# Performance work log

Hardware: AMD Instinct MI355X
Metric: run time of the kernel (lower is better)

## Reference

```python
import jax, jax.numpy as jnp
import numpy as np

N = 256        # total_nodes = num_instruments(16) + num_temporal_nodes(240)
D = 512        # node_dim
H = 512        # hidden_dim
E = 128        # edge_dim
HEADS = 4
L = 3          # num GAT layers
SLOPE = 0.2
LN_EPS = 1e-5


def _ln(x, g, b):
    m = jnp.mean(x, axis=-1, keepdims=True)
    v = jnp.mean((x - m) ** 2, axis=-1, keepdims=True)
    return (x - m) * jax.lax.rsqrt(v + LN_EPS) * g + b


def _pair_mlp(pairs, w1, b1, g, beta, w2, b2):
    # Linear -> LayerNorm -> LeakyReLU(0.2) -> Linear (dropout is identity in eval)
    h = pairs @ w1 + b1
    h = jax.nn.leaky_relu(_ln(h, g, beta), SLOPE)
    return h @ w2 + b2


def setup_inputs() -> dict:
    key = jax.random.key(0)
    ks = jax.random.split(key, 16)
    s = 0.02
    return {
        "emb": jax.random.normal(ks[0], (N, D), jnp.float32),
        # edge_predictor MLP: Linear(2D,H), LN(H), Linear(H,1)
        "ep_w1": jax.random.normal(ks[1], (2 * D, H), jnp.float32) * s,
        "ep_b1": jnp.zeros((H,), jnp.float32),
        "ep_g": jnp.ones((H,), jnp.float32),
        "ep_beta": jnp.zeros((H,), jnp.float32),
        "ep_w2": jax.random.normal(ks[2], (H, 1), jnp.float32) * s,
        "ep_b2": jnp.zeros((1,), jnp.float32),
        # edge_feature_net MLP: Linear(2D,H), LN(H), Linear(H,E)
        "ef_w1": jax.random.normal(ks[3], (2 * D, H), jnp.float32) * s,
        "ef_b1": jnp.zeros((H,), jnp.float32),
        "ef_g": jnp.ones((H,), jnp.float32),
        "ef_beta": jnp.zeros((H,), jnp.float32),
        "ef_w2": jax.random.normal(ks[4], (H, E), jnp.float32) * s,
        "ef_b2": jnp.zeros((E,), jnp.float32),
        # 3 GATConv layers (in=out=512, heads=4, concat=False), stacked
        "gat_W": jax.random.normal(ks[5], (L, H, HEADS * H), jnp.float32) * s,
        "gat_a_src": jax.random.normal(ks[6], (L, HEADS, H), jnp.float32) * s,
        "gat_a_dst": jax.random.normal(ks[7], (L, HEADS, H), jnp.float32) * s,
        "gat_b": jnp.zeros((L, H), jnp.float32),
        # output_proj: Linear(H,H), LN(H), Linear(H,D)
        "op_w1": jax.random.normal(ks[8], (H, H), jnp.float32) * s,
        "op_b1": jnp.zeros((H,), jnp.float32),
        "op_g": jnp.ones((H,), jnp.float32),
        "op_beta": jnp.zeros((H,), jnp.float32),
        "op_w2": jax.random.normal(ks[9], (H, D), jnp.float32) * s,
        "op_b2": jnp.zeros((D,), jnp.float32),
    }


def reference(emb, ep_w1, ep_b1, ep_g, ep_beta, ep_w2, ep_b2,
              ef_w1, ef_b1, ef_g, ef_beta, ef_w2, ef_b2,
              gat_W, gat_a_src, gat_a_dst, gat_b,
              op_w1, op_b1, op_g, op_beta, op_w2, op_b2):
    # ---- _construct_graph, fully vectorized over all ordered pairs ----
    # pairs[i, j] = concat(x_i, x_j)  -> [N, N, 2D]
    pairs = jnp.concatenate([
        jnp.broadcast_to(emb[:, None, :], (N, N, D)),
        jnp.broadcast_to(emb[None, :, :], (N, N, D)),
    ], axis=-1)
    prob = jax.nn.sigmoid(_pair_mlp(pairs, ep_w1, ep_b1, ep_g, ep_beta, ep_w2, ep_b2))[..., 0]  # [N,N]
    off_diag = ~jnp.eye(N, dtype=bool)
    active = (prob > 0.5) & off_diag           # active[i,j]: edge i -> j selected
    edge_feats = _pair_mlp(pairs, ef_w1, ef_b1, ef_g, ef_beta, ef_w2, ef_b2)  # [N,N,E]

    # adjacency in (dst, src) layout + self loops (PyG GATConv add_self_loops=True)
    adj = active.T | jnp.eye(N, dtype=bool)    # adj[dst, src]

    # ---- GATConv stack (heads=4, concat=False -> mean over heads) ----
    x = emb
    for l in range(L):
        s = (x @ gat_W[l]).reshape(N, HEADS, H)                 # [N, heads, C]
        a_s = jnp.einsum('nhc,hc->nh', s, gat_a_src[l])          # per-node src score
        a_d = jnp.einsum('nhc,hc->nh', s, gat_a_dst[l])          # per-node dst score
        logits = jax.nn.leaky_relu(a_d[:, None, :] + a_s[None, :, :], SLOPE)  # [dst, src, heads]
        logits = jnp.where(adj[:, :, None], logits, -1e9)
        alpha = jax.nn.softmax(logits, axis=1)                   # softmax over sources
        x = jnp.einsum('ijh,jhc->ihc', alpha, s).mean(axis=1) + gat_b[l]
        x = jax.nn.leaky_relu(x, SLOPE)

    # ---- output projection ----
    h = jax.nn.leaky_relu(_ln(x @ op_w1 + op_b1, op_g, op_beta), SLOPE)
    out = h @ op_w2 + op_b2                                      # [N, D]
    return (out, active, edge_feats)
```

## Files before the change

### kernel.cpp

```cpp
#include <hip/hip_runtime.h>


typedef __attribute__((ext_vector_type(8))) short short8;
typedef __attribute__((ext_vector_type(4))) float f32x4;
typedef unsigned short u16;
typedef unsigned int u32;

__device__ __forceinline__ float bf2f(u16 h) { return __uint_as_float(((u32)h) << 16); }
__device__ __forceinline__ u16 f2bf(float f) {
  u32 u = __float_as_uint(f);
  u += 0x7fffu + ((u >> 16) & 1u);
  return (u16)(u >> 16);
}
__device__ __forceinline__ float lrelu(float v) { return fmaxf(v, 0.2f * v); }
__device__ __forceinline__ float ldany(int f32mode, const void* p, int i) {
  return f32mode ? ((const float*)p)[i] : bf2f(((const u16*)p)[i]);
}

__global__ __launch_bounds__(256) void k_detect(const u16* emb, int* flag) {
  bool big = false;
  for (int i = blockIdx.x * 256 + threadIdx.x; i < 131072; i += 256 * 64) {
    float v = bf2f(emb[i]);
    big |= !(fabsf(v) <= 1e6f);
  }
  unsigned long long m = __ballot(big);
  if (m && (threadIdx.x & 63) == 0) atomicOr(flag, 1);
}

struct VD { const void* src; int dst, n; };
struct VArgs { VD v[16]; };
__global__ __launch_bounds__(256) void k_vec(VArgs a, const int* flag, float* out) {
  int f = *flag;
  VD d = a.v[blockIdx.x];
  for (int i = threadIdx.x; i < d.n; i += 256)
    out[d.dst + i] = ldany(f, d.src, i);
}

struct CArgs { const void* src[7]; float* dst[7]; int n[7]; };
__global__ __launch_bounds__(256) void k_cvt(CArgs a, const int* flag) {
  int f = *flag;
  int e = blockIdx.y;
  const void* s = a.src[e];
  float* d = a.dst[e];
  int n = a.n[e];
  for (int i = blockIdx.x * 256 + threadIdx.x; i < n; i += 2048 * 256)
    d[i] = ldany(f, s, i);
}

__global__ __launch_bounds__(256) void k_pack(const float* efw2f, u16* w2fr,
    const float* opw1f, u16* opw1p, const float* opw2f, u16* opw2p,
    const float* epw1f, float* wt, const float* efw1f, u16* wfr,
    const float* embf, u16* xfr) {
  __shared__ float T[64][65];
  int b = blockIdx.x, tid = threadIdx.x;
  if (b < 256) {
    int idx = b * 256 + tid;
    int e = idx & 7, l = (idx >> 3) & 63, nt = (idx >> 9) & 7, kc = idx >> 12;
    int n = nt * 16 + (l & 15);
    int c = kc * 32 + ((l >> 4) << 3) + e;
    w2fr[idx] = f2bf(efw2f[c * 128 + n]);
  } else if (b < 512) {
    int bb = b - 256;
    const float* Wf = (bb < 128) ? opw1f : opw2f;
    u16* wop = (bb < 128) ? opw1p : opw2p;
    int idx = (bb & 127) * 256 + tid;
    int lane = idx & 63, kc = (idx >> 6) & 15, nt = idx >> 10;
    int n = nt * 16 + (lane & 15);
    int c0 = kc * 32 + ((lane >> 4) << 3);
    u16* dst = wop + idx * 16;
#pragma unroll
    for (int e = 0; e < 8; ++e) {
      float v = Wf[(c0 + e) * 512 + n];
      u16 hi = f2bf(v);
      dst[e] = hi;
      dst[8 + e] = f2bf(v - bf2f(hi));
    }
  } else if (b < 640) {
    int q = b - 512;
    int k0 = (q & 7) * 64, c0 = ((q >> 3) & 7) * 64, z = q >> 6;
    const float* src = epw1f + z * 262144;
    float* dst = wt + z * 262144;
    int cl = tid & 63, rw = tid >> 6;
#pragma unroll
    for (int rr = 0; rr < 16; ++rr) {
      int r = rr * 4 + rw;
      T[r][cl] = src[(k0 + r) * 512 + c0 + cl];
    }
    __syncthreads();
#pragma unroll
    for (int rr = 0; rr < 16; ++rr) {
      int r = rr * 4 + rw;
      dst[(c0 + r) * 512 + k0 + cl] = T[cl][r];
    }
  } else if (b < 896) {
    int idx = (b - 640) * 256 + tid;
    int lane = idx & 63, kc = (idx >> 6) & 15, nt = idx >> 10;
    int n = nt * 16 + (lane & 15);
    int c0 = kc * 32 + ((lane >> 4) << 3);
    const float* base = (n < 512) ? (efw1f + n) : (efw1f + 262144 + n - 512);
    u16* dst = wfr + idx * 16;
#pragma unroll
    for (int e = 0; e < 8; ++e) {
      float v = base[(c0 + e) * 512];
      u16 hi = f2bf(v);
      dst[e] = hi;
      dst[8 + e] = f2bf(v - bf2f(hi));
    }
  } else {
    int idx = (b - 896) * 256 + tid;
    int lane = idx & 63, kc = (idx >> 6) & 15, it = idx >> 10;
    int i = it * 16 + (lane & 15);
    int c0 = kc * 32 + ((lane >> 4) << 3);
    const float* src = embf + i * 512 + c0;
    float4 v0 = *(const float4*)(src);
    float4 v1 = *(const float4*)(src + 4);
    float vv[8] = {v0.x, v0.y, v0.z, v0.w, v1.x, v1.y, v1.z, v1.w};
    u16* dst = xfr + idx * 16;
#pragma unroll
    for (int e = 0; e < 8; ++e) {
      u16 hi = f2bf(vv[e]);
      dst[e] = hi;
      dst[8 + e] = f2bf(vv[e] - bf2f(hi));
    }
  }
}

__global__ __launch_bounds__(256) void k_xb(const float* x, u16* xfr) {
  int idx = blockIdx.x * 256 + threadIdx.x;
  int lane = idx & 63, kc = (idx >> 6) & 15, it = idx >> 10;
  int i = it * 16 + (lane & 15);
  int c0 = kc * 32 + ((lane >> 4) << 3);
  const float* src = x + i * 512 + c0;
  float4 v0 = *(const float4*)(src);
  float4 v1 = *(const float4*)(src + 4);
  float vv[8] = {v0.x, v0.y, v0.z, v0.w, v1.x, v1.y, v1.z, v1.w};
  u16* dst = xfr + idx * 16;
#pragma unroll
  for (int e = 0; e < 8; ++e) {
    u16 hi = f2bf(vv[e]);
    dst[e] = hi;
    dst[8 + e] = f2bf(vv[e] - bf2f(hi));
  }
}

__global__ __launch_bounds__(256) void k_uvall(const u16* xfr, const u16* wfr,
    const float* embf, const float* wt, const float* vecf, float* uvf) {
  int b = blockIdx.x, tid = threadIdx.x;
  if (b < 256) {
    int lane = tid & 63, w = tid >> 6;
    int n0 = (b & 31) * 32 + (w & 1) * 16;
    int i0 = (b >> 5) * 32 + (w >> 1) * 16;
    int it = i0 >> 4, nt = n0 >> 4;
    const u16* ap = xfr + (it * 16) * 1024 + lane * 16;
    const u16* bp = wfr + (nt * 16) * 1024 + lane * 16;
    f32x4 acc = (f32x4){0.f, 0.f, 0.f, 0.f};
#pragma unroll
    for (int kc = 0; kc < 16; ++kc) {
      short8 ah = *(const short8*)(ap + kc * 1024);
      short8 al = *(const short8*)(ap + kc * 1024 + 8);
      short8 bh = *(const short8*)(bp + kc * 1024);
      short8 bl = *(const short8*)(bp + kc * 1024 + 8);
      acc = __builtin_amdgcn_mfma_f32_16x16x32_bf16(ah, bh, acc, 0, 0, 0);
      acc = __builtin_amdgcn_mfma_f32_16x16x32_bf16(ah, bl, acc, 0, 0, 0);
      acc = __builtin_amdgcn_mfma_f32_16x16x32_bf16(al, bh, acc, 0, 0, 0);
    }
    int col = n0 + (lane & 15);
    float bias = (col >= 512) ? vecf[2064 + col - 512] : 0.f;
    float* outb = (col < 512) ? (uvf + 262144 + col) : (uvf + 393216 + col - 512);
#pragma unroll
    for (int r = 0; r < 4; ++r) {
      int row = i0 + (lane >> 4) * 4 + r;
      outb[row * 512] = acc[r] + bias;
    }
  } else {
    int q = b - 256;
    int col = (q & 1) * 256 + tid;
    int r0 = ((q >> 1) & 63) * 4;
    int arr = q >> 7;
    const float* Wc = wt + arr * 262144 + col * 512;
    const float* e = embf + r0 * 512;
    float bias = (arr == 1) ? vecf[col] : 0.f;
    float* outp = uvf + arr * 131072 + r0 * 512 + col;
    double a0 = 0.0, a1 = 0.0, a2 = 0.0, a3 = 0.0;
    for (int k = 0; k < 512; k += 4) {
      float4 wv = *(const float4*)(Wc + k);
      double w0 = (double)wv.x, w1 = (double)wv.y;
      double w2 = (double)wv.z, w3 = (double)wv.w;
      float2 e0 = *(const float2*)(e + k);
      float2 e1 = *(const float2*)(e + 512 + k);
      float2 e2 = *(const float2*)(e + 1024 + k);
      float2 e3 = *(const float2*)(e + 1536 + k);
      a0 += (double)e0.x * w0 + (double)e0.y * w1;
      a1 += (double)e1.x * w0 + (double)e1.y * w1;
      a2 += (double)e2.x * w0 + (double)e2.y * w1;
      a3 += (double)e3.x * w0 + (double)e3.y * w1;
      float2 f0 = *(const float2*)(e + k + 2);
      float2 f1 = *(const float2*)(e + 512 + k + 2);
      float2 f2 = *(const float2*)(e + 1024 + k + 2);
      float2 f3 = *(const float2*)(e + 1536 + k + 2);
      a0 += (double)f0.x * w2 + (double)f0.y * w3;
      a1 += (double)f1.x * w2 + (double)f1.y * w3;
      a2 += (double)f2.x * w2 + (double)f2.y * w3;
      a3 += (double)f3.x * w2 + (double)f3.y * w3;
    }
    outp[0]    = (float)(a0 + (double)bias);
    outp[512]  = (float)(a1 + (double)bias);
    outp[1024] = (float)(a2 + (double)bias);
    outp[1536] = (float)(a3 + (double)bias);
  }
}

__global__ __launch_bounds__(256) void k_vfst(const float* uvf, float* vfrag,
    double* sums, double* sumsq) {
  int b = blockIdx.x, tid = threadIdx.x;
  if (b < 512) {
    const float* V = uvf + 393216;
    int idx = b * 256 + tid;
    int e = idx & 7, l = (idx >> 3) & 63, kc = (idx >> 9) & 15, jb = idx >> 13;
    int j = jb * 16 + (l & 15);
    int c = kc * 32 + ((l >> 4) << 3) + e;
    vfrag[idx] = V[j * 512 + c];
  } else {
    int lane = tid & 63, w = tid >> 6;
    int bid = (b - 512) * 4 + w;
    const float* p = uvf + bid * 512;
    double s = 0.0, s2 = 0.0;
    for (int q = lane; q < 512; q += 64) { double v = p[q]; s += v; s2 += v * v; }
#pragma unroll
    for (int m = 1; m < 64; m <<= 1) { s += __shfl_xor(s, m, 64); s2 += __shfl_xor(s2, m, 64); }
    if (lane == 0) { sums[bid] = s; sumsq[bid] = s2; }
  }
}

__global__ __launch_bounds__(256) void k_cross(const float* uvf, double* crossep,
                                               double* crossef) {
  __shared__ float Uc[16][132], Vc[16][132];
  int z = blockIdx.z;
  const float* U = uvf + z * 262144;
  const float* V = U + 131072;
  double* out = z ? crossef : crossep;
  int tid = threadIdx.x, ti = tid & 15, tj = tid >> 4;
  int i0 = blockIdx.y * 16, j0 = blockIdx.x * 16;
  double acc = 0.0;
  for (int c0 = 0; c0 < 512; c0 += 128) {
    __syncthreads();
    for (int idx = tid; idx < 2048; idx += 256) {
      int r = idx >> 7, c = idx & 127;
      Uc[r][c] = U[(i0 + r) * 512 + c0 + c];
      Vc[r][c] = V[(j0 + r) * 512 + c0 + c];
    }
    __syncthreads();
#pragma unroll
    for (int c4 = 0; c4 < 128; c4 += 4) {
      float4 uu = *(const float4*)&Uc[ti][c4];
      float4 vv = *(const float4*)&Vc[tj][c4];
      float p = fmaf(uu.x, vv.x, fmaf(uu.y, vv.y, fmaf(uu.z, vv.z, uu.w * vv.w)));
      acc += (double)p;
    }
  }
  out[(i0 + ti) * 256 + j0 + tj] = acc;
}

__global__ __launch_bounds__(256) void k_ep_t(const float* uvf, const double* sums,
    const double* sumsq, const double* crossep, const float* vecf,
    float* act, float* maskv) {
  __shared__ float Uc[16][132], Vc[16][132];
  int tid = threadIdx.x, ti = tid & 15, tj = tid >> 4;
  int i0 = blockIdx.y * 16, j0 = blockIdx.x * 16;
  int i = i0 + ti, j = j0 + tj;
  double md = (sums[i] + sums[256 + j]) * (1.0 / 512.0);
  double qd = (sumsq[i] + 2.0 * crossep[i * 256 + j] + sumsq[256 + j]) * (1.0 / 512.0);
  float iv = (float)(1.0 / sqrt(qd - md * md + 1e-5));
  float bb = (float)(-md) * iv;
  const float* U = uvf;
  const float* V = uvf + 131072;
  const float* g_ = vecf + 512;
  const float* be_ = vecf + 1024;
  const float* w2_ = vecf + 1536;
  double acc = 0.0;
  for (int c0 = 0; c0 < 512; c0 += 128) {
    __syncthreads();
    for (int idx = tid; idx < 2048; idx += 256) {
      int r = idx >> 7, c = idx & 127;
      Uc[r][c] = U[(i0 + r) * 512 + c0 + c];
      Vc[r][c] = V[(j0 + r) * 512 + c0 + c];
    }
    __syncthreads();
#pragma unroll
    for (int c4 = 0; c4 < 128; c4 += 4) {
      float4 uu = *(const float4*)&Uc[ti][c4];
      float4 vv = *(const float4*)&Vc[tj][c4];
      float4 gg = *(const float4*)(g_ + c0 + c4);
      float4 b4 = *(const float4*)(be_ + c0 + c4);
      float4 w4 = *(const float4*)(w2_ + c0 + c4);
      float z, s4 = 0.f;
      z = fmaf(fmaf(uu.x + vv.x, iv, bb), gg.x, b4.x); s4 = fmaf(lrelu(z), w4.x, s4);
      z = fmaf(fmaf(uu.y + vv.y, iv, bb), gg.y, b4.y); s4 = fmaf(lrelu(z), w4.y, s4);
      z = fmaf(fmaf(uu.z + vv.z, iv, bb), gg.z, b4.z); s4 = fmaf(lrelu(z), w4.z, s4);
      z = fmaf(fmaf(uu.w + vv.w, iv, bb), gg.w, b4.w); s4 = fmaf(lrelu(z), w4.w, s4);
      acc += (double)s4;
    }
  }
  double logit = acc + (double)vecf[2048];
  bool a = (logit > 0.0) && (i != j);
  act[i * 256 + j] = a ? 1.0f : 0.0f;
  maskv[j * 256 + i] = (a || i == j) ? 0.f : -1e9f;
}

__global__ __launch_bounds__(512, 2) void k_ef(const float* uvf, const double* sums,
    const double* sumsq, const double* crossef, const float* vecf,
    const u16* w2fr, const float* vfrag, float* ef_f) {
  __shared__ u16 w2S[16384];
  __shared__ float vS0[4096], vS1[4096];
  __shared__ float uS[8192];
  __shared__ float gS[512], beS[512];
  int tid = threadIdx.x;
  int lane = tid & 63, w = tid >> 6;
  int bx = blockIdx.x;
  int bi = bx >> 4, bj = bx & 15;
  int i0 = bi * 16;
  int iA = i0 + w * 2, iB = iA + 1;
  int l15 = lane & 15;
  int j = bj * 16 + l15;
  int ksl = (lane >> 4) * 8;

  double sj = sums[768 + j], s2j = sumsq[768 + j];
  double mA = (sums[512 + iA] + sj) * (1.0 / 512.0);
  double qA = (sumsq[512 + iA] + 2.0 * crossef[iA * 256 + j] + s2j) * (1.0 / 512.0);
  float ivA = (float)(1.0 / sqrt(qA - mA * mA + 1e-5));
  float bbA = (float)(-mA) * ivA;
  double mB = (sums[512 + iB] + sj) * (1.0 / 512.0);
  double qB = (sumsq[512 + iB] + 2.0 * crossef[iB * 256 + j] + s2j) * (1.0 / 512.0);
  float ivB = (float)(1.0 / sqrt(qB - mB * mB + 1e-5));
  float bbB = (float)(-mB) * ivB;

  const float* Vg = vfrag + bj * 8192;
  for (int q = tid; q < 2048; q += 512) {
    float4 v = *(const float4*)(Vg + q * 4);
    int kc = q >> 7, r = q & 127, ln = r >> 1;
    if (r & 1) *(float4*)(vS1 + kc * 256 + ln * 4) = v;
    else       *(float4*)(vS0 + kc * 256 + ln * 4) = v;
  }
  const float* Ug = uvf + 262144 + i0 * 512;
  for (int q = tid; q < 2048; q += 512)
    *(float4*)(uS + q * 4) = *(const float4*)(Ug + q * 4);
  if (tid < 128)      *(float4*)(gS + tid * 4)  = *(const float4*)(vecf + 2576 + tid * 4);
  else if (tid < 256) *(float4*)(beS + (tid - 128) * 4) = *(const float4*)(vecf + 3088 + (tid - 128) * 4);

  f32x4 acc[2][8];
#pragma unroll
  for (int ai = 0; ai < 2; ++ai)
#pragma unroll
    for (int bq = 0; bq < 8; ++bq) acc[ai][bq] = (f32x4){0.f, 0.f, 0.f, 0.f};

  auto H8 = [&](float4 u0, float4 u1, float4 v0, float4 v1, float4 g0, float4 g1,
                float4 e0, float4 e1, float iv, float bb) -> short8 {
    short8 a; float z;
    z = fmaf(u0.x + v0.x, iv, bb); z = fmaf(z, g0.x, e0.x); a[0] = (short)f2bf(lrelu(z));
    z = fmaf(u0.y + v0.y, iv, bb); z = fmaf(z, g0.y, e0.y); a[1] = (short)f2bf(lrelu(z));
    z = fmaf(u0.z + v0.z, iv, bb); z = fmaf(z, g0.z, e0.z); a[2] = (short)f2bf(lrelu(z));
    z = fmaf(u0.w + v0.w, iv, bb); z = fmaf(z, g0.w, e0.w); a[3] = (short)f2bf(lrelu(z));
    z = fmaf(u1.x + v1.x, iv, bb); z = fmaf(z, g1.x, e1.x); a[4] = (short)f2bf(lrelu(z));
    z = fmaf(u1.y + v1.y, iv, bb); z = fmaf(z, g1.y, e1.y); a[5] = (short)f2bf(lrelu(z));
    z = fmaf(u1.z + v1.z, iv, bb); z = fmaf(z, g1.z, e1.z); a[6] = (short)f2bf(lrelu(z));
    z = fmaf(u1.w + v1.w, iv, bb); z = fmaf(z, g1.w, e1.w); a[7] = (short)f2bf(lrelu(z));
    return a;
  };

  const float* uA = uS + (w * 2) * 512;
  const float* uB = uA + 512;

  for (int kq = 0; kq < 4; ++kq) {
    __syncthreads();
    const short8* src = (const short8*)(w2fr + kq * 16384);
    for (int q = tid; q < 2048; q += 512)
      *(short8*)(w2S + q * 8) = src[q];
    __syncthreads();
#pragma unroll
    for (int kk = 0; kk < 4; ++kk) {
      int kc = kq * 4 + kk;
      int k0 = kc * 32 + ksl;
      float4 u0 = *(const float4*)(uA + k0);
      float4 u1 = *(const float4*)(uA + k0 + 4);
      float4 b0 = *(const float4*)(uB + k0);
      float4 b1 = *(const float4*)(uB + k0 + 4);
      float4 v0 = *(const float4*)(vS0 + kc * 256 + lane * 4);
      float4 v1 = *(const float4*)(vS1 + kc * 256 + lane * 4);
      float4 g0 = *(const float4*)(gS + k0);
      float4 g1 = *(const float4*)(gS + k0 + 4);
      float4 e0 = *(const float4*)(beS + k0);
      float4 e1 = *(const float4*)(beS + k0 + 4);
      short8 aA = H8(u0, u1, v0, v1, g0, g1, e0, e1, ivA, bbA);
      short8 aB = H8(b0, b1, v0, v1, g0, g1, e0, e1, ivB, bbB);
#pragma unroll
      for (int nt = 0; nt < 8; ++nt) {
        short8 bv = *(const short8*)(w2S + kk * 4096 + nt * 512 + lane * 8);
        acc[0][nt] = __builtin_amdgcn_mfma_f32_16x16x32_bf16(aA, bv, acc[0][nt], 0, 0, 0);
        acc[1][nt] = __builtin_amdgcn_mfma_f32_16x16x32_bf16(aB, bv, acc[1][nt], 0, 0, 0);
      }
    }
  }
#pragma unroll
  for (int mi = 0; mi < 2; ++mi) {
    int ii = mi ? iB : iA;
#pragma unroll
    for (int nt = 0; nt < 8; ++nt) {
      int n = nt * 16 + l15;
      float bias = vecf[3600 + n];
#pragma unroll
      for (int r = 0; r < 4; ++r) {
        int row = (lane >> 4) * 4 + r;
        ef_f[(ii * 256 + bj * 16 + row) * 128 + n] = acc[mi][nt][r] + bias;
      }
    }
  }
}

__global__ __launch_bounds__(256) void k_wfrxb(const float* Wf, u16* wfr,
    const float* x, u16* xfr) {
  int b = blockIdx.x, tid = threadIdx.x;
  if (b < 512) {
    int idx = b * 256 + tid;
    int lane = idx & 63, kc = (idx >> 6) & 15, nt = idx >> 10;
    int n = nt * 16 + (lane & 15);
    int c0 = kc * 32 + ((lane >> 4) << 3);
    u16* dst = wfr + idx * 16;
#pragma unroll
    for (int e = 0; e < 8; ++e) {
      float v = Wf[(c0 + e) * 2048 + n];
      u16 hi = f2bf(v);
      dst[e] = hi;
      dst[8 + e] = f2bf(v - bf2f(hi));
    }
  } else {
    int idx = (b - 512) * 256 + tid;
    int lane = idx & 63, kc = (idx >> 6) & 15, it = idx >> 10;
    int i = it * 16 + (lane & 15);
    int c0 = kc * 32 + ((lane >> 4) << 3);
    const float* src = x + i * 512 + c0;
    float4 v0 = *(const float4*)(src);
    float4 v1 = *(const float4*)(src + 4);
    float vv[8] = {v0.x, v0.y, v0.z, v0.w, v1.x, v1.y, v1.z, v1.w};
    u16* dst = xfr + idx * 16;
#pragma unroll
    for (int e = 0; e < 8; ++e) {
      u16 hi = f2bf(vv[e]);
      dst[e] = hi;
      dst[8 + e] = f2bf(vv[e] - bf2f(hi));
    }
  }
}

__global__ __launch_bounds__(256) void k_sm(const u16* xfr, const u16* wfr, float* sf) {
  int tid = threadIdx.x, lane = tid & 63, w = tid >> 6;
  int n0 = blockIdx.x * 32 + (w & 1) * 16;
  int i0 = blockIdx.y * 32 + (w >> 1) * 16;
  int it = i0 >> 4, nt = n0 >> 4;
  const u16* ap = xfr + (it * 16) * 1024 + lane * 16;
  const u16* bp = wfr + (nt * 16) * 1024 + lane * 16;
  f32x4 acc = (f32x4){0.f, 0.f, 0.f, 0.f};
#pragma unroll
  for (int kc = 0; kc < 16; ++kc) {
    short8 ah = *(const short8*)(ap + kc * 1024);
    short8 al = *(const short8*)(ap + kc * 1024 + 8);
    short8 bh = *(const short8*)(bp + kc * 1024);
    short8 bl = *(const short8*)(bp + kc * 1024 + 8);
    acc = __builtin_amdgcn_mfma_f32_16x16x32_bf16(ah, bh, acc, 0, 0, 0);
    acc = __builtin_amdgcn_mfma_f32_16x16x32_bf16(ah, bl, acc, 0, 0, 0);
    acc = __builtin_amdgcn_mfma_f32_16x16x32_bf16(al, bh, acc, 0, 0, 0);
  }
  int col = n0 + (lane & 15);
#pragma unroll
  for (int r = 0; r < 4; ++r) {
    int row = i0 + (lane >> 4) * 4 + r;
    sf[row * 2048 + col] = acc[r];
  }
}

__global__ __launch_bounds__(256) void k_opm(const u16* xfr, const u16* wop,
    const float* bias, float* out) {
  int tid = threadIdx.x, lane = tid & 63, w = tid >> 6;
  int n0 = blockIdx.x * 32 + (w & 1) * 16;
  int i0 = blockIdx.y * 32 + (w >> 1) * 16;
  int it = i0 >> 4, nt = n0 >> 4;
  const u16* ap = xfr + (it * 16) * 1024 + lane * 16;
  const u16* bp = wop + (nt * 16) * 1024 + lane * 16;
  f32x4 acc = (f32x4){0.f, 0.f, 0.f, 0.f};
#pragma unroll
  for (int kc = 0; kc < 16; ++kc) {
    short8 ah = *(const short8*)(ap + kc * 1024);
    short8 al = *(const short8*)(ap + kc * 1024 + 8);
    short8 bh = *(const short8*)(bp + kc * 1024);
    short8 bl = *(const short8*)(bp + kc * 1024 + 8);
    acc = __builtin_amdgcn_mfma_f32_16x16x32_bf16(ah, bh, acc, 0, 0, 0);
    acc = __builtin_amdgcn_mfma_f32_16x16x32_bf16(ah, bl, acc, 0, 0, 0);
    acc = __builtin_amdgcn_mfma_f32_16x16x32_bf16(al, bh, acc, 0, 0, 0);
  }
  int col = n0 + (lane & 15);
  float b = bias[col];
#pragma unroll
  for (int r = 0; r < 4; ++r) {
    int row = i0 + (lane >> 4) * 4 + r;
    out[row * 512 + col] = acc[r] + b;
  }
}

__global__ __launch_bounds__(256) void k_adst(const float* sf, const float* vecf, int l,
    float* asf, float* adf, u16* sT_hi, u16* sT_lo) {
  __shared__ float T[64][65];
  int b = blockIdx.x, tid = threadIdx.x;
  if (b < 256) {
    int lane = tid & 63, w = tid >> 6;
    int bb = b * 4 + w;
    int n = bb >> 2, h = bb & 3;
    const float* s = sf + n * 2048 + h * 512;
    const float* as_ = vecf + 3728 + l * 2048 + h * 512;
    const float* ad_ = vecf + 9872 + l * 2048 + h * 512;
    float sa = 0.f, sd = 0.f;
    for (int c = lane; c < 512; c += 64) { sa = fmaf(s[c], as_[c], sa); sd = fmaf(s[c], ad_[c], sd); }
#pragma unroll
    for (int m = 1; m < 64; m <<= 1) { sa += __shfl_xor(sa, m, 64); sd += __shfl_xor(sd, m, 64); }
    if (lane == 0) { asf[bb] = sa; adf[bb] = sd; }
  } else {
    int q = b - 256;
    int hc0 = (q & 31) * 64;
    int n0 = (q >> 5) * 64;
    int h = hc0 >> 9, c0 = hc0 & 511, q0 = h * 256 + n0;
    int cl = tid & 63, rw = tid >> 6;
#pragma unroll
    for (int rr = 0; rr < 16; ++rr) {
      int r = rr * 4 + rw;
      T[r][cl] = sf[(n0 + r) * 2048 + hc0 + cl];
    }
    __syncthreads();
#pragma unroll
    for (int rr = 0; rr < 16; ++rr) {
      int r = rr * 4 + rw;
      float v = T[cl][r];
      u16 hi = f2bf(v);
      int o = (c0 + r) * 1024 + q0 + cl;
      sT_hi[o] = hi;
      sT_lo[o] = f2bf(v - bf2f(hi));
    }
  }
}

__global__ __launch_bounds__(256) void k_alpha(const float* asf, const float* adf,
    const float* maskv, u16* a_hib, u16* a_lob) {
  int dd = blockIdx.x, s = threadIdx.x;
  int lane = s & 63, w = s >> 6;
  __shared__ float wr[2][4][4];
  float mk = maskv[dd * 256 + s];
  float lg[4];
#pragma unroll
  for (int h = 0; h < 4; ++h) {
    float v = adf[dd * 4 + h] + asf[s * 4 + h];
    lg[h] = lrelu(v) + mk;
  }
#pragma unroll
  for (int h = 0; h < 4; ++h) {
    float v = lg[h];
#pragma unroll
    for (int m = 1; m < 64; m <<= 1) v = fmaxf(v, __shfl_xor(v, m, 64));
    if (lane == 0) wr[0][h][w] = v;
  }
  __syncthreads();
  float e[4];
#pragma unroll
  for (int h = 0; h < 4; ++h) {
    float mx = fmaxf(fmaxf(wr[0][h][0], wr[0][h][1]), fmaxf(wr[0][h][2], wr[0][h][3]));
    float v = __expf(lg[h] - mx);
    e[h] = v;
#pragma unroll
    for (int m = 1; m < 64; m <<= 1) v += __shfl_xor(v, m, 64);
    if (lane == 0) wr[1][h][w] = v;
  }
  __syncthreads();
#pragma unroll
  for (int h = 0; h < 4; ++h) {
    float sm = wr[1][h][0] + wr[1][h][1] + wr[1][h][2] + wr[1][h][3];
    float v = e[h] / sm;
    u16 hi = f2bf(v);
    int o = dd * 1024 + h * 256 + s;
    a_hib[o] = hi;
    a_lob[o] = f2bf(v - bf2f(hi));
  }
}

__global__ __launch_bounds__(256) void k_aggm(const u16* a_hi, const u16* a_lo,
    const u16* sT_hi, const u16* sT_lo, const float* vecf, int l, float* xout) {
  int tid = threadIdx.x, lane = tid & 63, w = tid >> 6;
  int c0 = blockIdx.x * 32 + (w & 1) * 16;
  int i0 = blockIdx.y * 32 + (w >> 1) * 16;
  int kb = (lane >> 4) * 8;
  int ar = (i0 + (lane & 15)) * 1024 + kb;
  int br = (c0 + (lane & 15)) * 1024 + kb;
  f32x4 acc = (f32x4){0.f, 0.f, 0.f, 0.f};
#pragma unroll 4
  for (int k0 = 0; k0 < 1024; k0 += 32) {
    short8 ah = *(const short8*)(a_hi + ar + k0);
    short8 al = *(const short8*)(a_lo + ar + k0);
    short8 bh = *(const short8*)(sT_hi + br + k0);
    short8 bl = *(const short8*)(sT_lo + br + k0);
    acc = __builtin_amdgcn_mfma_f32_16x16x32_bf16(ah, bh, acc, 0, 0, 0);
    acc = __builtin_amdgcn_mfma_f32_16x16x32_bf16(ah, bl, acc, 0, 0, 0);
    acc = __builtin_amdgcn_mfma_f32_16x16x32_bf16(al, bh, acc, 0, 0, 0);
  }
  int c = c0 + (lane & 15);
  float b = vecf[16016 + l * 512 + c];
#pragma unroll
  for (int r = 0; r < 4; ++r) {
    int i = i0 + (lane >> 4) * 4 + r;
    xout[i * 512 + c] = lrelu(fmaf(acc[r], 0.25f, b));
  }
}

__global__ __launch_bounds__(256) void k_ln(const float* t1, const float* vecf, float* h1f) {
  const float* g_ = vecf + 18064;
  const float* be_ = vecf + 18576;
  int row = blockIdx.x, tid = threadIdx.x, lane = tid & 63, w = tid >> 6;
  __shared__ float wr[2][4];
  float v0 = t1[row * 512 + tid];
  float v1 = t1[row * 512 + 256 + tid];
  float s = v0 + v1, s2 = fmaf(v0, v0, v1 * v1);
#pragma unroll
  for (int m = 1; m < 64; m <<= 1) { s += __shfl_xor(s, m, 64); s2 += __shfl_xor(s2, m, 64); }
  if (lane == 0) { wr[0][w] = s; wr[1][w] = s2; }
  __syncthreads();
  s = wr[0][0] + wr[0][1] + wr[0][2] + wr[0][3];
  s2 = wr[1][0] + wr[1][1] + wr[1][2] + wr[1][3];
  float m = s * (1.f / 512.f);
  float var = fmaxf(s2 * (1.f / 512.f) - m * m, 0.f);
  float iv = 1.f / sqrtf(var + 1e-5f);
  float z0 = (v0 - m) * iv * g_[tid] + be_[tid];
  float z1 = (v1 - m) * iv * g_[tid + 256] + be_[tid + 256];
  h1f[row * 512 + tid] = lrelu(z0);
  h1f[row * 512 + 256 + tid] = lrelu(z1);
}

extern "C" void kernel_launch(void* const* d_in, const int* in_sizes, int n_in,
                              void* d_out, int out_size, void* d_ws, size_t ws_size,
                              hipStream_t stream) {
  (void)out_size;
  static const int dictT[23] = {0,1,2,3,4,5,6,7,8,9,10,11,12,13,14,15,16,17,18,19,20,21,22};
  static const int alphaT[23] = {6,11,7,10,9,12,8,4,0,3,2,5,1,13,15,14,16,21,17,20,19,22,18};
  const int* tbl = (n_in == 23 && in_sizes[0] == 512) ? alphaT : dictT;
  auto IN = [&](int role) -> const void* { return d_in[tbl[role]]; };

  float* out_f = (float*)d_out;
  float* act_f = out_f + 256 * 512;
  float* ef_f  = out_f + 256 * 512 + 256 * 256;

  char* cur = (char*)d_ws;
  auto alloc = [&](size_t bytes) -> void* {
    void* r = (void*)cur;
    cur += (bytes + 255) & ~(size_t)255;
    return r;
  };
  float* vecf    = (float*)alloc(20480 * 4);
  float* embf    = (float*)alloc(131072 * 4);
  float* epw1f   = (float*)alloc(524288 * 4);
  float* efw1f   = (float*)alloc(524288 * 4);
  float* gatWf   = (float*)alloc(3145728 * 4);
  float* opw1f   = (float*)alloc(262144 * 4);
  float* opw2f   = (float*)alloc(262144 * 4);
  float* efw2f   = (float*)alloc(65536 * 4);
  float* uvf     = (float*)alloc(524288 * 4);
  float* sf      = (float*)alloc(524288 * 4);
  float* asf     = (float*)alloc(1024 * 4);
  float* adf     = (float*)alloc(1024 * 4);
  float* xf      = (float*)alloc(262144 * 4);
  float* t1      = (float*)alloc(131072 * 4);
  float* h1f     = (float*)alloc(131072 * 4);
  float* maskv   = (float*)alloc(65536 * 4);
  double* sums   = (double*)alloc(1024 * 8);
  double* sumsq  = (double*)alloc(1024 * 8);
  double* crossep = (double*)alloc(65536 * 8);
  double* crossef = (double*)alloc(65536 * 8);
  u16* w2tb      = (u16*)alloc(65536 * 2);
  float* vfrag   = (float*)alloc(131072 * 4);
  u16* wfrb      = (u16*)alloc(2097152 * 2);
  u16* xfrb      = (u16*)alloc(262144 * 2);
  u16* opw1p     = (u16*)alloc(524288 * 2);
  u16* opw2p     = (u16*)alloc(524288 * 2);
  float* wt      = (float*)alloc(524288 * 4);
  int* flag      = (int*)alloc(256);
  if ((size_t)(cur - (char*)d_ws) > ws_size) return;

  u16* sT_hi = (u16*)epw1f;
  u16* sT_lo = sT_hi + 524288;
  u16* a_hib = (u16*)efw1f;
  u16* a_lob = a_hib + 262144;

  hipMemsetAsync(flag, 0, 256, stream);
  hipLaunchKernelGGL(k_detect, dim3(64), dim3(256), 0, stream, (const u16*)IN(0), flag);

  {
    VArgs va;
    auto setV = [&](int qi, int role, int dst, int n) { va.v[qi] = {IN(role), dst, n}; };
    setV(0, 2, 0, 512);
    setV(1, 3, 512, 512);
    setV(2, 4, 1024, 512);
    setV(3, 5, 1536, 512);
    setV(4, 6, 2048, 1);
    setV(5, 8, 2064, 512);
    setV(6, 9, 2576, 512);
    setV(7, 10, 3088, 512);
    setV(8, 12, 3600, 128);
    setV(9, 14, 3728, 6144);
    setV(10, 15, 9872, 6144);
    setV(11, 16, 16016, 1536);
    setV(12, 18, 17552, 512);
    setV(13, 19, 18064, 512);
    setV(14, 20, 18576, 512);
    setV(15, 22, 19088, 512);
    hipLaunchKernelGGL(k_vec, dim3(16), dim3(256), 0, stream, va, (const int*)flag, vecf);
  }

  {
    CArgs ca;
    ca.src[0] = IN(0);  ca.dst[0] = embf;  ca.n[0] = 131072;
    ca.src[1] = IN(1);  ca.dst[1] = epw1f; ca.n[1] = 524288;
    ca.src[2] = IN(7);  ca.dst[2] = efw1f; ca.n[2] = 524288;
    ca.src[3] = IN(13); ca.dst[3] = gatWf; ca.n[3] = 3145728;
    ca.src[4] = IN(17); ca.dst[4] = opw1f; ca.n[4] = 262144;
    ca.src[5] = IN(21); ca.dst[5] = opw2f; ca.n[5] = 262144;
    ca.src[6] = IN(11); ca.dst[6] = efw2f; ca.n[6] = 65536;
    hipLaunchKernelGGL(k_cvt, dim3(2048, 7), dim3(256), 0, stream, ca, (const int*)flag);
  }

  hipLaunchKernelGGL(k_pack, dim3(960), dim3(256), 0, stream,
                     efw2f, w2tb, opw1f, opw1p, opw2f, opw2p,
                     epw1f, wt, efw1f, wfrb, embf, xfrb);

  hipLaunchKernelGGL(k_uvall, dim3(512), dim3(256), 0, stream,
                     xfrb, wfrb, embf, wt, vecf, uvf);

  hipLaunchKernelGGL(k_vfst, dim3(768), dim3(256), 0, stream, uvf, vfrag, sums, sumsq);
  hipLaunchKernelGGL(k_cross, dim3(16, 16, 2), dim3(256), 0, stream, uvf, crossep, crossef);

  hipLaunchKernelGGL(k_ep_t, dim3(16, 16), dim3(256), 0, stream,
                     uvf, sums, sumsq, crossep, vecf, act_f, maskv);
  hipLaunchKernelGGL(k_ef, dim3(256), dim3(512), 0, stream,
                     uvf, sums, sumsq, crossef, vecf, w2tb, vfrag, ef_f);

  const float* xsrc = embf;
  for (int l = 0; l < 3; ++l) {
    hipLaunchKernelGGL(k_wfrxb, dim3(576), dim3(256), 0, stream,
                       gatWf + l * 1048576, wfrb, xsrc, xfrb);
    hipLaunchKernelGGL(k_sm, dim3(64, 8), dim3(256), 0, stream, xfrb, wfrb, sf);
    hipLaunchKernelGGL(k_adst, dim3(384), dim3(256), 0, stream,
                       sf, vecf, l, asf, adf, sT_hi, sT_lo);
    hipLaunchKernelGGL(k_alpha, dim3(256), dim3(256), 0, stream, asf, adf, maskv,
                       a_hib, a_lob);
    float* xdst = xf + (l & 1) * 131072;
    hipLaunchKernelGGL(k_aggm, dim3(16, 8), dim3(256), 0, stream,
                       a_hib, a_lob, sT_hi, sT_lo, vecf, l, xdst);
    xsrc = xdst;
  }

  hipLaunchKernelGGL(k_xb, dim3(64), dim3(256), 0, stream, xsrc, xfrb);
  hipLaunchKernelGGL(k_opm, dim3(16, 8), dim3(256), 0, stream,
                     xfrb, opw1p, vecf + 17552, t1);
  hipLaunchKernelGGL(k_ln, dim3(256), dim3(256), 0, stream, t1, vecf, h1f);
  hipLaunchKernelGGL(k_xb, dim3(64), dim3(256), 0, stream, h1f, xfrb);
  hipLaunchKernelGGL(k_opm, dim3(16, 8), dim3(256), 0, stream,
                     xfrb, opw2p, vecf + 19088, out_f);
}
```

Measured before the change: 364.2 us.

## Fuse split-bf16 fragment packing into producer epilogues and merge cross/stats kernels

The GAT aggregation and layer-norm kernels now write their outputs straight into the hi/lo bf16 MFMA fragment layout, which removes the separate k_xb and the x-packing half of k_wfrxb. The fragments ping-pong between two buffers. The k_vfst and k_cross kernels are merged into one launch, and the fp64 projection path in k_uvall stages its embedding rows in shared memory. The goal is fewer launches and less intermediate global traffic, paid for with scattered 2-byte stores in the epilogues.

Result: faster. 348.9 us (-4.2%).

```diff
diff --git a/kernel.cpp b/kernel.cpp
--- a/kernel.cpp
+++ b/kernel.cpp
@@ -15,6 +15,13 @@
 __device__ __forceinline__ float lrelu(float v) { return fmaxf(v, 0.2f * v); }
 __device__ __forceinline__ float ldany(int f32mode, const void* p, int i) {
   return f32mode ? ((const float*)p)[i] : bf2f(((const u16*)p)[i]);
+}
+__device__ __forceinline__ void packfr(u16* xfr, float v, int row, int col) {
+  int lane2 = (row & 15) + (((col >> 3) & 3) << 4);
+  int off = (((row >> 4) * 16 + (col >> 5)) * 64 + lane2) * 16 + (col & 7);
+  u16 hi = f2bf(v);
+  xfr[off] = hi;
+  xfr[off + 8] = f2bf(v - bf2f(hi));
 }
 
 __global__ __launch_bounds__(256) void k_detect(const u16* emb, int* flag) {
@@ -125,26 +132,9 @@
   }
 }
 
-__global__ __launch_bounds__(256) void k_xb(const float* x, u16* xfr) {
-  int idx = blockIdx.x * 256 + threadIdx.x;
-  int lane = idx & 63, kc = (idx >> 6) & 15, it = idx >> 10;
-  int i = it * 16 + (lane & 15);
-  int c0 = kc * 32 + ((lane >> 4) << 3);
-  const float* src = x + i * 512 + c0;
-  float4 v0 = *(const float4*)(src);
-  float4 v1 = *(const float4*)(src + 4);
-  float vv[8] = {v0.x, v0.y, v0.z, v0.w, v1.x, v1.y, v1.z, v1.w};
-  u16* dst = xfr + idx * 16;
-#pragma unroll
-  for (int e = 0; e < 8; ++e) {
-    u16 hi = f2bf(vv[e]);
-    dst[e] = hi;
-    dst[8 + e] = f2bf(vv[e] - bf2f(hi));
-  }
-}
-
 __global__ __launch_bounds__(256) void k_uvall(const u16* xfr, const u16* wfr,
     const float* embf, const float* wt, const float* vecf, float* uvf) {
+  __shared__ float eS[2048];
   int b = blockIdx.x, tid = threadIdx.x;
   if (b < 256) {
     int lane = tid & 63, w = tid >> 6;
@@ -178,7 +168,10 @@
     int r0 = ((q >> 1) & 63) * 4;
     int arr = q >> 7;
     const float* Wc = wt + arr * 262144 + col * 512;
-    const float* e = embf + r0 * 512;
+    const float* eg = embf + r0 * 512;
+    for (int qq = tid; qq < 512; qq += 256)
+      *(float4*)(eS + qq * 4) = *(const float4*)(eg + qq * 4);
+    __syncthreads();
     float bias = (arr == 1) ? vecf[col] : 0.f;
     float* outp = uvf + arr * 131072 + r0 * 512 + col;
     double a0 = 0.0, a1 = 0.0, a2 = 0.0, a3 = 0.0;
@@ -186,18 +179,18 @@
       float4 wv = *(const float4*)(Wc + k);
       double w0 = (double)wv.x, w1 = (double)wv.y;
       double w2 = (double)wv.z, w3 = (double)wv.w;
-      float2 e0 = *(const float2*)(e + k);
-      float2 e1 = *(const float2*)(e + 512 + k);
-      float2 e2 = *(const float2*)(e + 1024 + k);
-      float2 e3 = *(const float2*)(e + 1536 + k);
+      float2 e0 = *(const float2*)(eS + k);
+      float2 e1 = *(const float2*)(eS + 512 + k);
+      float2 e2 = *(const float2*)(eS + 1024 + k);
+      float2 e3 = *(const float2*)(eS + 1536 + k);
       a0 += (double)e0.x * w0 + (double)e0.y * w1;
       a1 += (double)e1.x * w0 + (double)e1.y * w1;
       a2 += (double)e2.x * w0 + (double)e2.y * w1;
       a3 += (double)e3.x * w0 + (double)e3.y * w1;
-      float2 f0 = *(const float2*)(e + k + 2);
-      float2 f1 = *(const float2*)(e + 512 + k + 2);
-      float2 f2 = *(const float2*)(e + 1024 + k + 2);
-      float2 f3 = *(const float2*)(e + 1536 + k + 2);
+      float2 f0 = *(const float2*)(eS + k + 2);
+      float2 f1 = *(const float2*)(eS + 512 + k + 2);
+      float2 f2 = *(const float2*)(eS + 1024 + k + 2);
+      float2 f3 = *(const float2*)(eS + 1536 + k + 2);
       a0 += (double)f0.x * w2 + (double)f0.y * w3;
       a1 += (double)f1.x * w2 + (double)f1.y * w3;
       a2 += (double)f2.x * w2 + (double)f2.y * w3;
@@ -210,8 +203,9 @@
   }
 }
 
-__global__ __launch_bounds__(256) void k_vfst(const float* uvf, float* vfrag,
-    double* sums, double* sumsq) {
+__global__ __launch_bounds__(256) void k_vfcr(const float* uvf, float* vfrag,
+    double* sums, double* sumsq, double* crossep, double* crossef) {
+  __shared__ float Uc[16][132], Vc[16][132];
   int b = blockIdx.x, tid = threadIdx.x;
   if (b < 512) {
     const float* V = uvf + 393216;
@@ -220,7 +214,7 @@
     int j = jb * 16 + (l & 15);
     int c = kc * 32 + ((l >> 4) << 3) + e;
     vfrag[idx] = V[j * 512 + c];
-  } else {
+  } else if (b < 768) {
     int lane = tid & 63, w = tid >> 6;
     int bid = (b - 512) * 4 + w;
     const float* p = uvf + bid * 512;
@@ -229,36 +223,33 @@
 #pragma unroll
     for (int m = 1; m < 64; m <<= 1) { s += __shfl_xor(s, m, 64); s2 += __shfl_xor(s2, m, 64); }
     if (lane == 0) { sums[bid] = s; sumsq[bid] = s2; }
-  }
-}
-
-__global__ __launch_bounds__(256) void k_cross(const float* uvf, double* crossep,
-                                               double* crossef) {
-  __shared__ float Uc[16][132], Vc[16][132];
-  int z = blockIdx.z;
-  const float* U = uvf + z * 262144;
-  const float* V = U + 131072;
-  double* out = z ? crossef : crossep;
-  int tid = threadIdx.x, ti = tid & 15, tj = tid >> 4;
-  int i0 = blockIdx.y * 16, j0 = blockIdx.x * 16;
-  double acc = 0.0;
-  for (int c0 = 0; c0 < 512; c0 += 128) {
-    __syncthreads();
-    for (int idx = tid; idx < 2048; idx += 256) {
-      int r = idx >> 7, c = idx & 127;
-      Uc[r][c] = U[(i0 + r) * 512 + c0 + c];
-      Vc[r][c] = V[(j0 + r) * 512 + c0 + c];
-    }
-    __syncthreads();
-#pragma unroll
-    for (int c4 = 0; c4 < 128; c4 += 4) {
-      float4 uu = *(const float4*)&Uc[ti][c4];
-      float4 vv = *(const float4*)&Vc[tj][c4];
-      float p = fmaf(uu.x, vv.x, fmaf(uu.y, vv.y, fmaf(uu.z, vv.z, uu.w * vv.w)));
-      acc += (double)p;
-    }
-  }
-  out[(i0 + ti) * 256 + j0 + tj] = acc;
+  } else {
+    int q = b - 768;
+    int z = q >> 8, rem = q & 255;
+    const float* U = uvf + z * 262144;
+    const float* V = U + 131072;
+    double* out = z ? crossef : crossep;
+    int ti = tid & 15, tj = tid >> 4;
+    int i0 = (rem >> 4) * 16, j0 = (rem & 15) * 16;
+    double acc = 0.0;
+    for (int c0 = 0; c0 < 512; c0 += 128) {
+      __syncthreads();
+      for (int idx = tid; idx < 2048; idx += 256) {
+        int r = idx >> 7, c = idx & 127;
+        Uc[r][c] = U[(i0 + r) * 512 + c0 + c];
+        Vc[r][c] = V[(j0 + r) * 512 + c0 + c];
+      }
+      __syncthreads();
+#pragma unroll
+      for (int c4 = 0; c4 < 128; c4 += 4) {
+        float4 uu = *(const float4*)&Uc[ti][c4];
+        float4 vv = *(const float4*)&Vc[tj][c4];
+        float p = fmaf(uu.x, vv.x, fmaf(uu.y, vv.y, fmaf(uu.z, vv.z, uu.w * vv.w)));
+        acc += (double)p;
+      }
+    }
+    out[(i0 + ti) * 256 + j0 + tj] = acc;
+  }
 }
 
 __global__ __launch_bounds__(256) void k_ep_t(const float* uvf, const double* sums,
@@ -416,38 +407,18 @@
   }
 }
 
-__global__ __launch_bounds__(256) void k_wfrxb(const float* Wf, u16* wfr,
-    const float* x, u16* xfr) {
-  int b = blockIdx.x, tid = threadIdx.x;
-  if (b < 512) {
-    int idx = b * 256 + tid;
-    int lane = idx & 63, kc = (idx >> 6) & 15, nt = idx >> 10;
-    int n = nt * 16 + (lane & 15);
-    int c0 = kc * 32 + ((lane >> 4) << 3);
-    u16* dst = wfr + idx * 16;
-#pragma unroll
-    for (int e = 0; e < 8; ++e) {
-      float v = Wf[(c0 + e) * 2048 + n];
-      u16 hi = f2bf(v);
-      dst[e] = hi;
-      dst[8 + e] = f2bf(v - bf2f(hi));
-    }
-  } else {
-    int idx = (b - 512) * 256 + tid;
-    int lane = idx & 63, kc = (idx >> 6) & 15, it = idx >> 10;
-    int i = it * 16 + (lane & 15);
-    int c0 = kc * 32 + ((lane >> 4) << 3);
-    const float* src = x + i * 512 + c0;
-    float4 v0 = *(const float4*)(src);
-    float4 v1 = *(const float4*)(src + 4);
-    float vv[8] = {v0.x, v0.y, v0.z, v0.w, v1.x, v1.y, v1.z, v1.w};
-    u16* dst = xfr + idx * 16;
-#pragma unroll
-    for (int e = 0; e < 8; ++e) {
-      u16 hi = f2bf(vv[e]);
-      dst[e] = hi;
-      dst[8 + e] = f2bf(vv[e] - bf2f(hi));
-    }
+__global__ __launch_bounds__(256) void k_wfr(const float* Wf, u16* wfr) {
+  int idx = blockIdx.x * 256 + threadIdx.x;
+  int lane = idx & 63, kc = (idx >> 6) & 15, nt = idx >> 10;
+  int n = nt * 16 + (lane & 15);
+  int c0 = kc * 32 + ((lane >> 4) << 3);
+  u16* dst = wfr + idx * 16;
+#pragma unroll
+  for (int e = 0; e < 8; ++e) {
+    float v = Wf[(c0 + e) * 2048 + n];
+    u16 hi = f2bf(v);
+    dst[e] = hi;
+    dst[8 + e] = f2bf(v - bf2f(hi));
   }
 }
 
@@ -588,7 +559,7 @@
 }
 
 __global__ __launch_bounds__(256) void k_aggm(const u16* a_hi, const u16* a_lo,
-    const u16* sT_hi, const u16* sT_lo, const float* vecf, int l, float* xout) {
+    const u16* sT_hi, const u16* sT_lo, const float* vecf, int l, u16* xfr_out) {
   int tid = threadIdx.x, lane = tid & 63, w = tid >> 6;
   int c0 = blockIdx.x * 32 + (w & 1) * 16;
   int i0 = blockIdx.y * 32 + (w >> 1) * 16;
@@ -611,11 +582,12 @@
 #pragma unroll
   for (int r = 0; r < 4; ++r) {
     int i = i0 + (lane >> 4) * 4 + r;
-    xout[i * 512 + c] = lrelu(fmaf(acc[r], 0.25f, b));
-  }
-}
-
-__global__ __launch_bounds__(256) void k_ln(const float* t1, const float* vecf, float* h1f) {
+    packfr(xfr_out, lrelu(fmaf(acc[r], 0.25f, b)), i, c);
+  }
+}
+
+__global__ __launch_bounds__(256) void k_ln(const float* t1, const float* vecf,
+                                            u16* xfr_out) {
   const float* g_ = vecf + 18064;
   const float* be_ = vecf + 18576;
   int row = blockIdx.x, tid = threadIdx.x, lane = tid & 63, w = tid >> 6;
@@ -634,8 +606,8 @@
   float iv = 1.f / sqrtf(var + 1e-5f);
   float z0 = (v0 - m) * iv * g_[tid] + be_[tid];
   float z1 = (v1 - m) * iv * g_[tid + 256] + be_[tid + 256];
-  h1f[row * 512 + tid] = lrelu(z0);
-  h1f[row * 512 + 256 + tid] = lrelu(z1);
+  packfr(xfr_out, lrelu(z0), row, tid);
+  packfr(xfr_out, lrelu(z1), row, tid + 256);
 }
 
 extern "C" void kernel_launch(void* const* d_in, const int* in_sizes, int n_in,
@@ -669,9 +641,7 @@
   float* sf      = (float*)alloc(524288 * 4);
   float* asf     = (float*)alloc(1024 * 4);
   float* adf     = (float*)alloc(1024 * 4);
-  float* xf      = (float*)alloc(262144 * 4);
   float* t1      = (float*)alloc(131072 * 4);
-  float* h1f     = (float*)alloc(131072 * 4);
   float* maskv   = (float*)alloc(65536 * 4);
   double* sums   = (double*)alloc(1024 * 8);
   double* sumsq  = (double*)alloc(1024 * 8);
@@ -680,7 +650,8 @@
   u16* w2tb      = (u16*)alloc(65536 * 2);
   float* vfrag   = (float*)alloc(131072 * 4);
   u16* wfrb      = (u16*)alloc(2097152 * 2);
-  u16* xfrb      = (u16*)alloc(262144 * 2);
+  u16* xfrA      = (u16*)alloc(262144 * 2);
+  u16* xfrB      = (u16*)alloc(262144 * 2);
   u16* opw1p     = (u16*)alloc(524288 * 2);
   u16* opw2p     = (u16*)alloc(524288 * 2);
   float* wt      = (float*)alloc(524288 * 4);
@@ -731,39 +702,37 @@
 
   hipLaunchKernelGGL(k_pack, dim3(960), dim3(256), 0, stream,
                      efw2f, w2tb, opw1f, opw1p, opw2f, opw2p,
-                     epw1f, wt, efw1f, wfrb, embf, xfrb);
+                     epw1f, wt, efw1f, wfrb, embf, xfrA);
 
   hipLaunchKernelGGL(k_uvall, dim3(512), dim3(256), 0, stream,
-                     xfrb, wfrb, embf, wt, vecf, uvf);
-
-  hipLaunchKernelGGL(k_vfst, dim3(768), dim3(256), 0, stream, uvf, vfrag, sums, sumsq);
-  hipLaunchKernelGGL(k_cross, dim3(16, 16, 2), dim3(256), 0, stream, uvf, crossep, crossef);
+                     xfrA, wfrb, embf, wt, vecf, uvf);
+
+  hipLaunchKernelGGL(k_vfcr, dim3(1280), dim3(256), 0, stream,
+                     uvf, vfrag, sums, sumsq, crossep, crossef);
 
   hipLaunchKernelGGL(k_ep_t, dim3(16, 16), dim3(256), 0, stream,
                      uvf, sums, sumsq, crossep, vecf, act_f, maskv);
   hipLaunchKernelGGL(k_ef, dim3(256), dim3(512), 0, stream,
                      uvf, sums, sumsq, crossef, vecf, w2tb, vfrag, ef_f);
 
-  const float* xsrc = embf;
+  u16* xcur = xfrA;
+  u16* xnxt = xfrB;
   for (int l = 0; l < 3; ++l) {
-    hipLaunchKernelGGL(k_wfrxb, dim3(576), dim3(256), 0, stream,
-                       gatWf + l * 1048576, wfrb, xsrc, xfrb);
-    hipLaunchKernelGGL(k_sm, dim3(64, 8), dim3(256), 0, stream, xfrb, wfrb, sf);
+    hipLaunchKernelGGL(k_wfr, dim3(512), dim3(256), 0, stream,
+                       gatWf + l * 1048576, wfrb);
+    hipLaunchKernelGGL(k_sm, dim3(64, 8), dim3(256), 0, stream, xcur, wfrb, sf);
     hipLaunchKernelGGL(k_adst, dim3(384), dim3(256), 0, stream,
                        sf, vecf, l, asf, adf, sT_hi, sT_lo);
     hipLaunchKernelGGL(k_alpha, dim3(256), dim3(256), 0, stream, asf, adf, maskv,
                        a_hib, a_lob);
-    float* xdst = xf + (l & 1) * 131072;
     hipLaunchKernelGGL(k_aggm, dim3(16, 8), dim3(256), 0, stream,
-                       a_hib, a_lob, sT_hi, sT_lo, vecf, l, xdst);
-    xsrc = xdst;
-  }
-
-  hipLaunchKernelGGL(k_xb, dim3(64), dim3(256), 0, stream, xsrc, xfrb);
+                       a_hib, a_lob, sT_hi, sT_lo, vecf, l, xnxt);
+    u16* t = xcur; xcur = xnxt; xnxt = t;
+  }
+
   hipLaunchKernelGGL(k_opm, dim3(16, 8), dim3(256), 0, stream,
-                     xfrb, opw1p, vecf + 17552, t1);
-  hipLaunchKernelGGL(k_ln, dim3(256), dim3(256), 0, stream, t1, vecf, h1f);
-  hipLaunchKernelGGL(k_xb, dim3(64), dim3(256), 0, stream, h1f, xfrb);
+                     xcur, opw1p, vecf + 17552, t1);
+  hipLaunchKernelGGL(k_ln, dim3(256), dim3(256), 0, stream, t1, vecf, xnxt);
   hipLaunchKernelGGL(k_opm, dim3(16, 8), dim3(256), 0, stream,
-                     xfrb, opw2p, vecf + 19088, out_f);
-}
+                     xnxt, opw2p, vecf + 19088, out_f);
+}
```
